# Kernel tuning notes

Hardware: AMD Instinct MI355X
Metric: run time of the kernel (lower is better)

## Reference

```python
import jax, jax.numpy as jnp
import numpy as np

VOCAB = 100000
EMB = 256
HID = 512
HH = HID // 2  # per-direction hidden
NTAGS = 12
START_IDX = 10
STOP_IDX = 11
NEG = -10000.0


def setup_inputs() -> dict:
    key = jax.random.key(0)
    ks = jax.random.split(key, 12)
    B, T = 32, 256
    sentence = jax.random.randint(ks[0], (B, T), 0, VOCAB)
    h0 = jax.random.normal(ks[1], (2, B, HH), jnp.float32)
    c0 = jax.random.normal(ks[2], (2, B, HH), jnp.float32)
    embed = jax.random.normal(ks[3], (VOCAB, EMB), jnp.float32) * 0.1
    W_ih_f = jax.random.normal(ks[4], (4 * HH, EMB), jnp.float32) * 0.05
    W_hh_f = jax.random.normal(ks[5], (4 * HH, HH), jnp.float32) * 0.05
    b_f = jnp.zeros((4 * HH,), jnp.float32)
    W_ih_b = jax.random.normal(ks[6], (4 * HH, EMB), jnp.float32) * 0.05
    W_hh_b = jax.random.normal(ks[7], (4 * HH, HH), jnp.float32) * 0.05
    b_b = jnp.zeros((4 * HH,), jnp.float32)
    W_out = jax.random.normal(ks[8], (NTAGS, HID), jnp.float32) * 0.05
    b_out = jnp.zeros((NTAGS,), jnp.float32)
    transitions = jax.random.normal(ks[9], (NTAGS, NTAGS), jnp.float32)
    transitions = transitions.at[START_IDX, :].set(NEG)
    transitions = transitions.at[:, STOP_IDX].set(NEG)
    return {"sentence": sentence, "embed": embed,
            "W_ih_f": W_ih_f, "W_hh_f": W_hh_f, "b_f": b_f,
            "W_ih_b": W_ih_b, "W_hh_b": W_hh_b, "b_b": b_b,
            "W_out": W_out, "b_out": b_out,
            "transitions": transitions, "h0": h0, "c0": c0}


def _lstm_dir(xs, h0, c0, W_ih, W_hh, b, reverse):
    # xs: [T, B, E] -> hs: [T, B, HH]
    def step(carry, x):
        h, c = carry
        z = x @ W_ih.T + h @ W_hh.T + b
        i, f, g, o = jnp.split(z, 4, axis=-1)
        c = jax.nn.sigmoid(f) * c + jax.nn.sigmoid(i) * jnp.tanh(g)
        h = jax.nn.sigmoid(o) * jnp.tanh(c)
        return (h, c), h
    _, hs = jax.lax.scan(step, (h0, c0), xs, reverse=reverse)
    return hs


def _viterbi_single(feats, transitions):
    # feats: [T, NTAGS]
    init = jnp.full((NTAGS,), NEG, feats.dtype).at[START_IDX].set(0.0)

    def step(fv, emit):
        m = fv[None, :] + transitions          # [next, prev]
        bp = jnp.argmax(m, axis=1)             # best prev per next tag
        fv_new = jnp.max(m, axis=1) + emit
        return fv_new, bp

    fv, bps = jax.lax.scan(step, init, feats)
    terminal = fv + transitions[STOP_IDX]
    best = jnp.argmax(terminal)
    score = terminal[best]

    def back(tag, bp):
        return bp[tag], tag
    _, path = jax.lax.scan(back, best, bps, reverse=True)
    return score, path


def reference(sentence, embed, W_ih_f, W_hh_f, b_f, W_ih_b, W_hh_b, b_b,
              W_out, b_out, transitions, h0, c0):
    # sentence: [B, T] -> embeds [T, B, E]
    xs = embed[sentence.T]
    hf = _lstm_dir(xs, h0[0], c0[0], W_ih_f, W_hh_f, b_f, reverse=False)
    hb = _lstm_dir(xs, h0[1], c0[1], W_ih_b, W_hh_b, b_b, reverse=True)
    lstm_out = jnp.concatenate([hf, hb], axis=-1)           # [T, B, HID]
    feats = lstm_out @ W_out.T + b_out                      # [T, B, NTAGS]
    feats_bt = jnp.transpose(feats, (1, 0, 2))              # [B, T, NTAGS]
    scores, paths = jax.vmap(_viterbi_single, in_axes=(0, None))(feats_bt, transitions)
    return scores, paths
```

## Files before the change

### kernel.cpp

```cpp
#include <hip/hip_runtime.h>
#include <math.h>

#define T_LEN  256
#define BATCH  32
#define EMBD   256
#define HHD    256
#define NTAGS  12
#define NEGV   (-10000.0f)

__global__ __launch_bounds__(256) void gemm_zx(
    const int* __restrict__ sentence, const float* __restrict__ embed,
    const float* __restrict__ Wf,  const float* __restrict__ Wb,
    const float* __restrict__ bf,  const float* __restrict__ bb,
    float* __restrict__ zx)
{
    __shared__ float As[16][132];
    __shared__ float Bs[16][132];

    const int tid = threadIdx.x;
    const int tx = tid & 15, ty = tid >> 4;
    const int Mbase = (int)(blockIdx.x >> 4) * 128;
    const int Nbase = (int)(blockIdx.x & 15) * 128;

    const float* Wsrc = (Nbase < 1024) ? Wf : Wb;
    const float* bsrc = (Nbase < 1024) ? bf : bb;
    const int nOff = (Nbase < 1024) ? Nbase : (Nbase - 1024);

    const int m0 = tid >> 2;
    const int m1 = m0 + 64;
    const int kq = (tid & 3) * 4;
    const int mg0 = Mbase + m0, mg1 = Mbase + m1;
    const int tok0 = sentence[(mg0 & 31) * T_LEN + (mg0 >> 5)];
    const int tok1 = sentence[(mg1 & 31) * T_LEN + (mg1 >> 5)];
    const float* arow0 = embed + (long long)tok0 * EMBD;
    const float* arow1 = embed + (long long)tok1 * EMBD;
    const float* brow0 = Wsrc + (long long)(nOff + m0) * EMBD;
    const float* brow1 = Wsrc + (long long)(nOff + m1) * EMBD;

    float acc[8][8];
#pragma unroll
    for (int i = 0; i < 8; ++i)
#pragma unroll
        for (int j = 0; j < 8; ++j) acc[i][j] = 0.0f;

    for (int k0 = 0; k0 < EMBD; k0 += 16) {
        float4 av0 = *(const float4*)(arow0 + k0 + kq);
        float4 av1 = *(const float4*)(arow1 + k0 + kq);
        float4 bv0 = *(const float4*)(brow0 + k0 + kq);
        float4 bv1 = *(const float4*)(brow1 + k0 + kq);
        __syncthreads();
        As[kq+0][m0] = av0.x; As[kq+1][m0] = av0.y; As[kq+2][m0] = av0.z; As[kq+3][m0] = av0.w;
        As[kq+0][m1] = av1.x; As[kq+1][m1] = av1.y; As[kq+2][m1] = av1.z; As[kq+3][m1] = av1.w;
        Bs[kq+0][m0] = bv0.x; Bs[kq+1][m0] = bv0.y; Bs[kq+2][m0] = bv0.z; Bs[kq+3][m0] = bv0.w;
        Bs[kq+0][m1] = bv1.x; Bs[kq+1][m1] = bv1.y; Bs[kq+2][m1] = bv1.z; Bs[kq+3][m1] = bv1.w;
        __syncthreads();
#pragma unroll
        for (int kt = 0; kt < 16; ++kt) {
            float am[8], bn[8];
            *(float4*)&am[0] = *(const float4*)&As[kt][ty * 4];
            *(float4*)&am[4] = *(const float4*)&As[kt][64 + ty * 4];
            *(float4*)&bn[0] = *(const float4*)&Bs[kt][tx * 4];
            *(float4*)&bn[4] = *(const float4*)&Bs[kt][64 + tx * 4];
#pragma unroll
            for (int i = 0; i < 8; ++i)
#pragma unroll
                for (int j = 0; j < 8; ++j) acc[i][j] += am[i] * bn[j];
        }
    }

    float4 bias0 = *(const float4*)(bsrc + nOff + tx * 4);
    float4 bias1 = *(const float4*)(bsrc + nOff + 64 + tx * 4);
    const float bnv[8] = {bias0.x, bias0.y, bias0.z, bias0.w,
                          bias1.x, bias1.y, bias1.z, bias1.w};
#pragma unroll
    for (int i = 0; i < 8; ++i) {
        const int mg = Mbase + ty * 4 + (i & 3) + ((i >= 4) ? 64 : 0);
        float4 o0 = make_float4(acc[i][0] + bnv[0], acc[i][1] + bnv[1],
                                acc[i][2] + bnv[2], acc[i][3] + bnv[3]);
        float4 o1 = make_float4(acc[i][4] + bnv[4], acc[i][5] + bnv[5],
                                acc[i][6] + bnv[6], acc[i][7] + bnv[7]);
        *(float4*)(zx + (long long)mg * 2048 + Nbase + tx * 4) = o0;
        *(float4*)(zx + (long long)mg * 2048 + Nbase + 64 + tx * 4) = o1;
    }
}

__global__ __launch_bounds__(256) void pack_whh(
    const float* __restrict__ Whf, const float* __restrict__ Whb,
    float* __restrict__ pack)
{
    const int gid = blockIdx.x * 256 + threadIdx.x;
    const int k2   = gid & 127;
    const int j    = (gid >> 7) & 255;
    const int half = (gid >> 15) & 1;
    const int q    = (gid >> 16) & 3;
    const int d    = (gid >> 18) & 1;
    const float* W = d ? Whb : Whf;
    const int g = j >> 6;
    const int e = q * 64 + (j & 63);
    pack[gid] = W[(g * 256 + e) * 256 + half * 128 + k2];
}

__global__ __launch_bounds__(512, 2) void lstm_team(
    const float* __restrict__ zx, const float* __restrict__ pack,
    const float* __restrict__ h0, const float* __restrict__ c0,
    unsigned long long* __restrict__ hx,
    float* __restrict__ lstm_out)
{
    __shared__ float hS0[256];
    __shared__ float hS1[256];
    __shared__ float pS[512];

    const int tid = threadIdx.x;
    const int bx  = (int)blockIdx.x;
    const int q = bx & 3, d = (bx >> 2) & 1, b = bx >> 3;

    float4 wreg[32];
    {
        const float4* wrow = (const float4*)(pack + ((long long)(bx & 7) << 16)
                                             + tid * 128);
#pragma unroll
        for (int c = 0; c < 32; ++c) wreg[c] = wrow[c];
    }
#pragma unroll
    for (int c = 0; c < 32; ++c) {
        asm volatile("" : "+v"(wreg[c].x), "+v"(wreg[c].y),
                          "+v"(wreg[c].z), "+v"(wreg[c].w));
    }

    const int half = tid >> 8;
    const long long hxbase = (long long)(d * 32 + b) * 256;
    const long long zbase = (long long)d * 1024 + q * 64 + (tid & 63);
    float creg = (tid < 64) ? c0[(d * 32 + b) * 256 + q * 64 + tid] : 0.0f;

    if (tid < 256) hS0[tid] = h0[(d * 32 + b) * 256 + tid];
    __syncthreads();

    for (int s = 0; s < T_LEN; ++s) {
        const int t = d ? (T_LEN - 1 - s) : s;

        float zv0 = 0.f, zv1 = 0.f, zv2 = 0.f, zv3 = 0.f;
        if (tid < 64) {
            const float* zr = zx + (long long)(t * 32 + b) * 2048 + zbase;
            zv0 = zr[0]; zv1 = zr[256]; zv2 = zr[512]; zv3 = zr[768];
        }

        const float* h  = (s & 1) ? hS1 : hS0;
        float*       hN = (s & 1) ? hS0 : hS1;
        const float* hh = h + half * 128;

        float a = 0.0f;
#pragma unroll
        for (int c = 0; c < 32; ++c) {
            const float4 hv = *(const float4*)(hh + c * 4);
            a += wreg[c].x * hv.x + wreg[c].y * hv.y
               + wreg[c].z * hv.z + wreg[c].w * hv.w;
        }
        pS[tid] = a;
        __syncthreads();

        const int parN = (s & 1) ^ 1;
        if (tid < 64) {
            const float zi = pS[tid]       + pS[tid + 256] + zv0;
            const float zf = pS[tid + 64]  + pS[tid + 320] + zv1;
            const float zg = pS[tid + 128] + pS[tid + 384] + zv2;
            const float zo = pS[tid + 192] + pS[tid + 448] + zv3;
            const float si = 1.0f / (1.0f + expf(-zi));
            const float sf = 1.0f / (1.0f + expf(-zf));
            const float so = 1.0f / (1.0f + expf(-zo));
            creg = sf * creg + si * tanhf(zg);
            const float hn = so * tanhf(creg);
            const int e = q * 64 + tid;
            hN[e] = hn;
            lstm_out[(long long)(t * 32 + b) * 512 + d * 256 + e] = hn;
            __hip_atomic_store(hx + (long long)parN * 16384 + hxbase + e,
                ((unsigned long long)(unsigned)(s + 1) << 32)
                    | (unsigned long long)__float_as_uint(hn),
                __ATOMIC_RELAXED, __HIP_MEMORY_SCOPE_AGENT);
        } else if (s < T_LEN - 1) {
            int e = -1;
            if (tid < 256) { if ((tid >> 6) != q) e = tid; }
            else if (tid < 320) { if (q != 0) e = tid - 256; }
            if (e >= 0) {
                const unsigned long long* slot =
                    hx + (long long)parN * 16384 + hxbase + e;
                unsigned long long v;
                do {
                    v = __hip_atomic_load(slot, __ATOMIC_RELAXED,
                                          __HIP_MEMORY_SCOPE_AGENT);
                } while ((unsigned)(v >> 32) != (unsigned)(s + 1));
                hN[e] = __uint_as_float((unsigned)v);
            }
        }
        __syncthreads();
    }
}

__global__ __launch_bounds__(256) void feats_kernel(
    const float* __restrict__ lstm_out, const float* __restrict__ W_out,
    const float* __restrict__ b_out, float* __restrict__ feats)
{
    const int gid = blockIdx.x * 256 + threadIdx.x;
    if (gid >= 8192 * NTAGS) return;
    const int row = gid / NTAGS;
    const int tag = gid - row * NTAGS;
    const float4* x = (const float4*)(lstm_out + (long long)row * 512);
    const float4* w = (const float4*)(W_out + (long long)tag * 512);
    float acc = b_out[tag];
#pragma unroll 4
    for (int k = 0; k < 128; ++k) {
        float4 a = x[k], bw = w[k];
        acc += a.x * bw.x + a.y * bw.y + a.z * bw.z + a.w * bw.w;
    }
    const int t = row >> 5, b = row & 31;
    feats[(long long)b * (T_LEN * NTAGS) + t * NTAGS + tag] = acc;
}

__global__ __launch_bounds__(64) void viterbi_kernel(
    const float* __restrict__ feats, const float* __restrict__ trans,
    float* __restrict__ out)
{
    __shared__ float featS[T_LEN * NTAGS];
    __shared__ float transS[NTAGS * NTAGS];
    __shared__ float fvS[NTAGS];
    __shared__ unsigned char bpS[T_LEN][NTAGS];
    __shared__ float pathS[T_LEN];

    const int b = blockIdx.x;
    const int lane = threadIdx.x;

    {
        const float4* src = (const float4*)(feats + (long long)b * (T_LEN * NTAGS));
        float4* dst = (float4*)featS;
        for (int i = lane; i < (T_LEN * NTAGS) / 4; i += 64) dst[i] = src[i];
        for (int i = lane; i < NTAGS * NTAGS; i += 64) transS[i] = trans[i];
    }
    __syncthreads();

    float fv[NTAGS];
#pragma unroll
    for (int p = 0; p < NTAGS; ++p) fv[p] = (p == 10) ? 0.0f : NEGV;

    for (int t = 0; t < T_LEN; ++t) {
        if (lane < NTAGS) {
            float best = -3.4e38f; int bi = 0;
#pragma unroll
            for (int p = 0; p < NTAGS; ++p) {
                const float v = fv[p] + transS[lane * NTAGS + p];
                if (v > best) { best = v; bi = p; }
            }
            bpS[t][lane] = (unsigned char)bi;
            fvS[lane] = best + featS[t * NTAGS + lane];
        }
        __syncthreads();
#pragma unroll
        for (int p = 0; p < NTAGS; ++p) fv[p] = fvS[p];
        __syncthreads();
    }

    if (lane < NTAGS) fvS[lane] = fv[lane] + transS[11 * NTAGS + lane];
    __syncthreads();
    if (lane == 0) {
        float best = -3.4e38f; int bi = 0;
        for (int p = 0; p < NTAGS; ++p) {
            const float v = fvS[p];
            if (v > best) { best = v; bi = p; }
        }
        out[b] = best;
        int cur = bi;
        pathS[T_LEN - 1] = (float)cur;
        for (int tt = T_LEN - 2; tt >= 0; --tt) {
            cur = bpS[tt + 1][cur];
            pathS[tt] = (float)cur;
        }
    }
    __syncthreads();
    float* po = out + BATCH + (long long)b * T_LEN;
    for (int i = lane; i < T_LEN; i += 64) po[i] = pathS[i];
}

extern "C" void kernel_launch(void* const* d_in, const int* in_sizes, int n_in,
                              void* d_out, int out_size, void* d_ws, size_t ws_size,
                              hipStream_t stream)
{
    (void)in_sizes; (void)n_in; (void)out_size; (void)ws_size;
    const int*   sentence = (const int*)  d_in[0];
    const float* embed    = (const float*)d_in[1];
    const float* W_ih_f   = (const float*)d_in[2];
    const float* W_hh_f   = (const float*)d_in[3];
    const float* b_f      = (const float*)d_in[4];
    const float* W_ih_b   = (const float*)d_in[5];
    const float* W_hh_b   = (const float*)d_in[6];
    const float* b_b      = (const float*)d_in[7];
    const float* W_out    = (const float*)d_in[8];
    const float* b_out    = (const float*)d_in[9];
    const float* trans    = (const float*)d_in[10];
    const float* h0       = (const float*)d_in[11];
    const float* c0       = (const float*)d_in[12];
    float* out = (float*)d_out;

    char* ws = (char*)d_ws;
    float* zx       = (float*)ws; ws += (long long)8192 * 2048 * 4;
    float* lstm_out = (float*)ws; ws += (long long)8192 * 512 * 4;
    float* feats    = (float*)ws; ws += BATCH * T_LEN * NTAGS * 4;
    float* pack     = (float*)ws; ws += (long long)524288 * 4;
    unsigned long long* hx = (unsigned long long*)ws; ws += 2 * 16384 * 8;

    pack_whh<<<2048, 256, 0, stream>>>(W_hh_f, W_hh_b, pack);
    gemm_zx<<<1024, 256, 0, stream>>>(sentence, embed, W_ih_f, W_ih_b, b_f, b_b, zx);
    lstm_team<<<256, 512, 0, stream>>>(zx, pack, h0, c0, hx, lstm_out);
    feats_kernel<<<384, 256, 0, stream>>>(lstm_out, W_out, b_out, feats);
    viterbi_kernel<<<32, 64, 0, stream>>>(feats, trans, out);
}
```

Measured before the change: 895.4 us.

## Remap LSTM team blocks across XCDs and add fast-path sc0 spin polling

Changes the block-to-(batch, quarter, direction) mapping so that the four blocks cooperating on one batch/direction sit 8 blocks apart, likely landing them on the same XCD under round-robin dispatch and sharing an L2. It also adds a second exchange buffer written with a plain volatile store, which consumers poll using inline global_load_dwordx2 with sc0. They fall back to the agent-scope atomic buffer if the fast poll does not see the value within 1024 tries. The aim is lower inter-block handoff latency per timestep, at the cost of relying on the hardware dispatch order and cache behaviour.

Result: slower. 1.069 ms (+19.4%).

```diff
diff --git a/kernel.cpp b/kernel.cpp
--- a/kernel.cpp
+++ b/kernel.cpp
@@ -103,7 +103,8 @@
 __global__ __launch_bounds__(512, 2) void lstm_team(
     const float* __restrict__ zx, const float* __restrict__ pack,
     const float* __restrict__ h0, const float* __restrict__ c0,
-    unsigned long long* __restrict__ hx,
+    unsigned long long* __restrict__ hxF,
+    unsigned long long* __restrict__ hxS,
     float* __restrict__ lstm_out)
 {
     __shared__ float hS0[256];
@@ -112,11 +113,14 @@
 
     const int tid = threadIdx.x;
     const int bx  = (int)blockIdx.x;
-    const int q = bx & 3, d = (bx >> 2) & 1, b = bx >> 3;
+    const int b  = ((bx >> 5) & 3) * 8 + (bx & 7);
+    const int q  = (bx >> 3) & 3;
+    const int d  = (bx >> 7) & 1;
+    const int sl = d * 4 + q;
 
     float4 wreg[32];
     {
-        const float4* wrow = (const float4*)(pack + ((long long)(bx & 7) << 16)
+        const float4* wrow = (const float4*)(pack + ((long long)sl << 16)
                                              + tid * 128);
 #pragma unroll
         for (int c = 0; c < 32; ++c) wreg[c] = wrow[c];
@@ -131,6 +135,7 @@
     const long long hxbase = (long long)(d * 32 + b) * 256;
     const long long zbase = (long long)d * 1024 + q * 64 + (tid & 63);
     float creg = (tid < 64) ? c0[(d * 32 + b) * 256 + q * 64 + tid] : 0.0f;
+    int fastOK = 1;
 
     if (tid < 256) hS0[tid] = h0[(d * 32 + b) * 256 + tid];
     __syncthreads();
@@ -172,22 +177,41 @@
             const int e = q * 64 + tid;
             hN[e] = hn;
             lstm_out[(long long)(t * 32 + b) * 512 + d * 256 + e] = hn;
-            __hip_atomic_store(hx + (long long)parN * 16384 + hxbase + e,
+            const unsigned long long tv =
                 ((unsigned long long)(unsigned)(s + 1) << 32)
-                    | (unsigned long long)__float_as_uint(hn),
-                __ATOMIC_RELAXED, __HIP_MEMORY_SCOPE_AGENT);
+                    | (unsigned long long)__float_as_uint(hn);
+            const long long off = (long long)parN * 16384 + hxbase + e;
+            *(volatile unsigned long long*)(hxF + off) = tv;
+            __hip_atomic_store(hxS + off, tv, __ATOMIC_RELAXED,
+                               __HIP_MEMORY_SCOPE_AGENT);
         } else if (s < T_LEN - 1) {
             int e = -1;
             if (tid < 256) { if ((tid >> 6) != q) e = tid; }
             else if (tid < 320) { if (q != 0) e = tid - 256; }
             if (e >= 0) {
-                const unsigned long long* slot =
-                    hx + (long long)parN * 16384 + hxbase + e;
+                const long long off = (long long)parN * 16384 + hxbase + e;
                 unsigned long long v;
-                do {
-                    v = __hip_atomic_load(slot, __ATOMIC_RELAXED,
-                                          __HIP_MEMORY_SCOPE_AGENT);
-                } while ((unsigned)(v >> 32) != (unsigned)(s + 1));
+                int got = 0;
+                if (fastOK) {
+                    const unsigned long long* sf_p = hxF + off;
+                    for (int it = 0; it < 1024; ++it) {
+                        asm volatile(
+                            "global_load_dwordx2 %0, %1, off sc0\n\t"
+                            "s_waitcnt vmcnt(0)"
+                            : "=&v"(v) : "v"(sf_p) : "memory");
+                        if ((unsigned)(v >> 32) == (unsigned)(s + 1)) {
+                            got = 1; break;
+                        }
+                    }
+                    if (!got) fastOK = 0;
+                }
+                if (!got) {
+                    const unsigned long long* ss_p = hxS + off;
+                    do {
+                        v = __hip_atomic_load(ss_p, __ATOMIC_RELAXED,
+                                              __HIP_MEMORY_SCOPE_AGENT);
+                    } while ((unsigned)(v >> 32) != (unsigned)(s + 1));
+                }
                 hN[e] = __uint_as_float((unsigned)v);
             }
         }
@@ -303,11 +327,12 @@
     float* lstm_out = (float*)ws; ws += (long long)8192 * 512 * 4;
     float* feats    = (float*)ws; ws += BATCH * T_LEN * NTAGS * 4;
     float* pack     = (float*)ws; ws += (long long)524288 * 4;
-    unsigned long long* hx = (unsigned long long*)ws; ws += 2 * 16384 * 8;
+    unsigned long long* hxS = (unsigned long long*)ws; ws += 2 * 16384 * 8;
+    unsigned long long* hxF = (unsigned long long*)ws; ws += 2 * 16384 * 8;
 
     pack_whh<<<2048, 256, 0, stream>>>(W_hh_f, W_hh_b, pack);
     gemm_zx<<<1024, 256, 0, stream>>>(sentence, embed, W_ih_f, W_ih_b, b_f, b_b, zx);
-    lstm_team<<<256, 512, 0, stream>>>(zx, pack, h0, c0, hx, lstm_out);
+    lstm_team<<<256, 512, 0, stream>>>(zx, pack, h0, c0, hxF, hxS, lstm_out);
     feats_kernel<<<384, 256, 0, stream>>>(lstm_out, W_out, b_out, feats);
     viterbi_kernel<<<32, 64, 0, stream>>>(feats, trans, out);
 }
```

## Prefetch next-step gate inputs, remap LSTM blocks, and pin weight registers

Applied to the files above, without the earlier changes.

Each LSTM step now issues the global loads of the next timestep's precomputed input-gate values before the recurrent dot product, so their latency overlaps the current step's compute and the cross-block h exchange. The block index mapping changes so that blocks sharing a weight slice are grouped differently across the grid. Launch bounds drop from two blocks per CU to one, and the weight registers are pinned inside every loop iteration, both meant to stop the compiler spilling or rematerialising the 128 weight floats. The risks are higher register pressure and the dependence of the spin-wait exchange on block placement.

Result: faster. 785.0 us (-12.3%).

```diff
diff --git a/kernel.cpp b/kernel.cpp
--- a/kernel.cpp
+++ b/kernel.cpp
@@ -7,6 +7,23 @@
 #define HHD    256
 #define NTAGS  12
 #define NEGV   (-10000.0f)
+
+#define PIN4(r0,r1,r2,r3)                                                  \
+    asm volatile("" : "+v"(r0.x),"+v"(r0.y),"+v"(r0.z),"+v"(r0.w),         \
+                      "+v"(r1.x),"+v"(r1.y),"+v"(r1.z),"+v"(r1.w),         \
+                      "+v"(r2.x),"+v"(r2.y),"+v"(r2.z),"+v"(r2.w),         \
+                      "+v"(r3.x),"+v"(r3.y),"+v"(r3.z),"+v"(r3.w))
+
+#define PIN_ALL_W() do {                                                   \
+    PIN4(wreg[0],wreg[1],wreg[2],wreg[3]);                                 \
+    PIN4(wreg[4],wreg[5],wreg[6],wreg[7]);                                 \
+    PIN4(wreg[8],wreg[9],wreg[10],wreg[11]);                               \
+    PIN4(wreg[12],wreg[13],wreg[14],wreg[15]);                             \
+    PIN4(wreg[16],wreg[17],wreg[18],wreg[19]);                             \
+    PIN4(wreg[20],wreg[21],wreg[22],wreg[23]);                             \
+    PIN4(wreg[24],wreg[25],wreg[26],wreg[27]);                             \
+    PIN4(wreg[28],wreg[29],wreg[30],wreg[31]);                             \
+} while (0)
 
 __global__ __launch_bounds__(256) void gemm_zx(
     const int* __restrict__ sentence, const float* __restrict__ embed,
@@ -100,7 +117,7 @@
     pack[gid] = W[(g * 256 + e) * 256 + half * 128 + k2];
 }
 
-__global__ __launch_bounds__(512, 2) void lstm_team(
+__global__ __launch_bounds__(512, 1) void lstm_team(
     const float* __restrict__ zx, const float* __restrict__ pack,
     const float* __restrict__ h0, const float* __restrict__ c0,
     unsigned long long* __restrict__ hx,
@@ -112,36 +129,44 @@
 
     const int tid = threadIdx.x;
     const int bx  = (int)blockIdx.x;
-    const int q = bx & 3, d = (bx >> 2) & 1, b = bx >> 3;
+    const int b  = ((bx >> 5) & 3) * 8 + (bx & 7);
+    const int q  = (bx >> 3) & 3;
+    const int d  = (bx >> 7) & 1;
+    const int sl = d * 4 + q;
 
     float4 wreg[32];
     {
-        const float4* wrow = (const float4*)(pack + ((long long)(bx & 7) << 16)
+        const float4* wrow = (const float4*)(pack + ((long long)sl << 16)
                                              + tid * 128);
 #pragma unroll
         for (int c = 0; c < 32; ++c) wreg[c] = wrow[c];
     }
-#pragma unroll
-    for (int c = 0; c < 32; ++c) {
-        asm volatile("" : "+v"(wreg[c].x), "+v"(wreg[c].y),
-                          "+v"(wreg[c].z), "+v"(wreg[c].w));
-    }
+    PIN_ALL_W();
 
     const int half = tid >> 8;
     const long long hxbase = (long long)(d * 32 + b) * 256;
-    const long long zbase = (long long)d * 1024 + q * 64 + (tid & 63);
     float creg = (tid < 64) ? c0[(d * 32 + b) * 256 + q * 64 + tid] : 0.0f;
 
     if (tid < 256) hS0[tid] = h0[(d * 32 + b) * 256 + tid];
     __syncthreads();
 
+    const int zco = d * 1024 + q * 64 + (tid & 63);
+    float zv0 = 0.f, zv1 = 0.f, zv2 = 0.f, zv3 = 0.f;
+    if (tid < 64) {
+        const int t0 = d ? (T_LEN - 1) : 0;
+        const float* zr = zx + (long long)(t0 * 32 + b) * 2048 + zco;
+        zv0 = zr[0]; zv1 = zr[256]; zv2 = zr[512]; zv3 = zr[768];
+    }
+
     for (int s = 0; s < T_LEN; ++s) {
+        PIN_ALL_W();
         const int t = d ? (T_LEN - 1 - s) : s;
 
-        float zv0 = 0.f, zv1 = 0.f, zv2 = 0.f, zv3 = 0.f;
-        if (tid < 64) {
-            const float* zr = zx + (long long)(t * 32 + b) * 2048 + zbase;
-            zv0 = zr[0]; zv1 = zr[256]; zv2 = zr[512]; zv3 = zr[768];
+        float zn0 = zv0, zn1 = zv1, zn2 = zv2, zn3 = zv3;
+        if (tid < 64 && s < T_LEN - 1) {
+            const int tn = d ? (T_LEN - 2 - s) : (s + 1);
+            const float* zr = zx + (long long)(tn * 32 + b) * 2048 + zco;
+            zn0 = zr[0]; zn1 = zr[256]; zn2 = zr[512]; zn3 = zr[768];
         }
 
         const float* h  = (s & 1) ? hS1 : hS0;
@@ -191,6 +216,7 @@
                 hN[e] = __uint_as_float((unsigned)v);
             }
         }
+        zv0 = zn0; zv1 = zn1; zv2 = zn2; zv3 = zn3;
         __syncthreads();
     }
 }
```
